# Kernel optimization log

Measured on AMD Instinct MI355X. Metric: run time of the kernel, lower is better.

The kernel has to match this reference:

```python
import jax, jax.numpy as jnp
import numpy as np
from jax import lax

B, T, D = 1, 2048, 2048
H, KVH, HD = 16, 4, 128
BETA = 0.9
ROPE_BASE = 10000.0


def _causal_prefix_ema(x, beta):
    # x: (B, T, D); m_t = beta * m_{t-1} + (1 - beta) * x_t, m_{-1} = 0
    def step(m, xt):
        m = beta * m + (1.0 - beta) * xt
        return m, m
    _, ys = lax.scan(step, jnp.zeros_like(x[:, 0]), jnp.swapaxes(x, 0, 1))
    return jnp.swapaxes(ys, 0, 1)


def _rotate_half(x):
    x1, x2 = jnp.split(x, 2, axis=-1)
    return jnp.concatenate([-x2, x1], axis=-1)


def _rope_cos_sin(t, hd, dtype):
    inv_freq = 1.0 / (ROPE_BASE ** (jnp.arange(0, hd, 2, dtype=jnp.float32) / hd))
    freqs = jnp.arange(t, dtype=jnp.float32)[:, None] * inv_freq[None, :]  # (T, HD/2)
    emb = jnp.concatenate([freqs, freqs], axis=-1)  # (T, HD)
    return jnp.cos(emb).astype(dtype)[None, None], jnp.sin(emb).astype(dtype)[None, None]


def setup_inputs() -> dict:
    key = jax.random.key(0)
    ks = jax.random.split(key, 8)
    std = 0.02
    return {
        "hidden_states": jax.random.normal(ks[0], (B, T, D), jnp.float32),
        "Wq": jax.random.normal(ks[1], (D, H * HD), jnp.float32) * std,
        "Wk": jax.random.normal(ks[2], (D, KVH * HD), jnp.float32) * std,
        "Wv": jax.random.normal(ks[3], (D, KVH * HD), jnp.float32) * std,
        "Wo": jax.random.normal(ks[4], (H * HD, D), jnp.float32) * std,
        "Wr1": jax.random.normal(ks[5], (D, D // 2), jnp.float32) * std,
        "br1": jnp.zeros((D // 2,), jnp.float32),
        "Wr2": jax.random.normal(ks[6], (D // 2, 2), jnp.float32) * std,
        "br2": jnp.zeros((2,), jnp.float32),
    }


def reference(hidden_states, Wq, Wk, Wv, Wo, Wr1, br1, Wr2, br2):
    b, t, d = hidden_states.shape
    q = hidden_states @ Wq  # (B, T, H*HD)

    # multi-level memories: l1 = raw, l2 = causal prefix EMA
    l2 = _causal_prefix_ema(hidden_states, BETA)

    # router MLP on q + softmax over levels
    h = jax.nn.silu(q @ Wr1 + br1)
    lam = jax.nn.softmax(h @ Wr2 + br2, axis=-1)  # (B, T, 2)
    fused = lam[..., 0:1] * hidden_states + lam[..., 1:2] * l2

    # shape to heads
    q_s = q.reshape(b, t, H, HD).transpose(0, 2, 1, 3)                 # (B, H, T, HD)
    k_s = (fused @ Wk).reshape(b, t, KVH, HD).transpose(0, 2, 1, 3)    # (B, KVH, T, HD)
    v_s = (fused @ Wv).reshape(b, t, KVH, HD).transpose(0, 2, 1, 3)

    # RoPE
    cos, sin = _rope_cos_sin(t, HD, q_s.dtype)
    q_s = q_s * cos + _rotate_half(q_s) * sin
    k_s = k_s * cos + _rotate_half(k_s) * sin

    # repeat kv for GQA
    n_rep = H // KVH
    k_s = jnp.repeat(k_s, n_rep, axis=1)
    v_s = jnp.repeat(v_s, n_rep, axis=1)

    # causal SDPA
    scale = 1.0 / jnp.sqrt(jnp.asarray(HD, q_s.dtype))
    scores = jnp.einsum("bhqd,bhkd->bhqk", q_s, k_s) * scale
    causal = jnp.tril(jnp.ones((t, t), dtype=bool))
    scores = jnp.where(causal[None, None], scores, jnp.finfo(scores.dtype).min)
    attn = jax.nn.softmax(scores, axis=-1)
    out = jnp.einsum("bhqk,bhkd->bhqd", attn, v_s)  # (B, H, T, HD)

    out = out.transpose(0, 2, 1, 3).reshape(b, t, H * HD)
    return out @ Wo
```

## Files before the change

### kernel.cpp

```cpp
#include <hip/hip_runtime.h>
#include <hip/hip_bf16.h>

#define T_SEQ 2048
#define D_MODEL 2048
#define NH 16
#define NKVH 4
#define HD 128

typedef __attribute__((ext_vector_type(8))) short bf16x8;
typedef __attribute__((ext_vector_type(4))) float f32x4;

static __device__ __forceinline__ short f32_to_bf16(float f) {
    unsigned u = __float_as_uint(f);
    u += 0x7fffu + ((u >> 16) & 1u);
    return (short)(u >> 16);
}
static __device__ __forceinline__ float bf16_to_f32(short s) {
    return __uint_as_float(((unsigned)(unsigned short)s) << 16);
}
static __device__ __forceinline__ void gl_to_lds16(const void* g, void* l) {
    __builtin_amdgcn_global_load_lds(
        (const __attribute__((address_space(1))) unsigned int*)g,
        (__attribute__((address_space(3))) unsigned int*)l, 16, 0, 0);
}

template<int BM>
__global__ __launch_bounds__(256) void gemm_bt_kernel(
    const short* __restrict__ A, const short* __restrict__ Bt,
    float* __restrict__ Cf, short* __restrict__ Cb,
    int M, int N, int K, const float* __restrict__ bias, int act)
{
    constexpr int NI = (BM == 128) ? 4 : 2;
    constexpr int ACH = BM / 32;
    __shared__ short Alds[2][BM * 64];
    __shared__ short Blds[2][128 * 64];

    const int tid = threadIdx.x;
    const int wave = tid >> 6, lane = tid & 63;
    const int l16 = lane & 15, quad = lane >> 4;
    const int wm = (BM == 128) ? (wave >> 1) * 64 : 0;
    const int wn = (BM == 128) ? (wave & 1) * 64 : wave * 32;
    const int m0 = blockIdx.y * BM, n0 = blockIdx.x * 128;
    const int niter = K >> 6;

    f32x4 acc[4][NI] = {};

    #pragma unroll
    for (int p = 0; p < ACH; ++p) {
        int li = p * 256 + tid;
        int row = li >> 3, sc = li & 7;
        gl_to_lds16(A + (size_t)(m0 + row) * K + ((sc ^ (row & 7)) * 8),
                    &Alds[0][(size_t)(p * 256 + wave * 64) * 8]);
    }
    #pragma unroll
    for (int p = 0; p < 4; ++p) {
        int li = p * 256 + tid;
        int row = li >> 3, sc = li & 7;
        gl_to_lds16(Bt + (size_t)(n0 + row) * K + ((sc ^ (row & 7)) * 8),
                    &Blds[0][(size_t)(p * 256 + wave * 64) * 8]);
    }

    for (int t = 0; t < niter; ++t) {
        asm volatile("s_waitcnt vmcnt(0)\n\ts_barrier" ::: "memory");

        if (t + 1 < niter) {
            int k1 = (t + 1) << 6;
            int nb = (t + 1) & 1;
            #pragma unroll
            for (int p = 0; p < ACH; ++p) {
                int li = p * 256 + tid;
                int row = li >> 3, sc = li & 7;
                gl_to_lds16(A + (size_t)(m0 + row) * K + k1 + ((sc ^ (row & 7)) * 8),
                            &Alds[nb][(size_t)(p * 256 + wave * 64) * 8]);
            }
            #pragma unroll
            for (int p = 0; p < 4; ++p) {
                int li = p * 256 + tid;
                int row = li >> 3, sc = li & 7;
                gl_to_lds16(Bt + (size_t)(n0 + row) * K + k1 + ((sc ^ (row & 7)) * 8),
                            &Blds[nb][(size_t)(p * 256 + wave * 64) * 8]);
            }
        }

        const short* Ab = Alds[t & 1];
        const short* Bb = Blds[t & 1];
        #pragma unroll
        for (int kk = 0; kk < 2; ++kk) {
            bf16x8 a[4], b[NI];
            #pragma unroll
            for (int i = 0; i < 4; ++i)
                a[i] = *(const bf16x8*)
                    &Ab[(size_t)(wm + i * 16 + l16) * 64 + (((kk * 4 + quad) ^ (l16 & 7)) * 8)];
            #pragma unroll
            for (int i = 0; i < NI; ++i)
                b[i] = *(const bf16x8*)
                    &Bb[(size_t)(wn + i * 16 + l16) * 64 + (((kk * 4 + quad) ^ (l16 & 7)) * 8)];
            #pragma unroll
            for (int mi = 0; mi < 4; ++mi)
                #pragma unroll
                for (int ni = 0; ni < NI; ++ni)
                    acc[mi][ni] = __builtin_amdgcn_mfma_f32_16x16x32_bf16(
                        a[mi], b[ni], acc[mi][ni], 0, 0, 0);
        }
    }

    #pragma unroll
    for (int mi = 0; mi < 4; ++mi) {
        #pragma unroll
        for (int ni = 0; ni < NI; ++ni) {
            int col = n0 + wn + ni * 16 + l16;
            float bv = bias ? bias[col] : 0.0f;
            #pragma unroll
            for (int r = 0; r < 4; ++r) {
                int row = m0 + wm + mi * 16 + quad * 4 + r;
                float x = acc[mi][ni][r] + bv;
                if (act) x = x / (1.0f + __expf(-x));
                size_t o = (size_t)row * N + col;
                if (Cf) Cf[o] = x;
                if (Cb) Cb[o] = f32_to_bf16(x);
            }
        }
    }
}

__global__ __launch_bounds__(256) void transpose_all_kernel(
    const float* __restrict__ Wq, const float* __restrict__ Wk,
    const float* __restrict__ Wv, const float* __restrict__ Wr1,
    const float* __restrict__ Wo, short* __restrict__ Wq_t,
    short* __restrict__ Wkv_t, short* __restrict__ Wr1_t,
    short* __restrict__ Wo_t)
{
    __shared__ float tile[32][33];
    int bx = blockIdx.x;
    const float* src; short* dst; int ld, cb;
    if (bx < 64)       { src = Wq;  dst = Wq_t;  ld = 2048; cb = bx; }
    else if (bx < 80)  { src = Wk;  dst = Wkv_t; ld = 512;  cb = bx - 64; }
    else if (bx < 96)  { src = Wv;  dst = Wkv_t + (size_t)512 * 2048; ld = 512; cb = bx - 80; }
    else if (bx < 128) { src = Wr1; dst = Wr1_t; ld = 1024; cb = bx - 96; }
    else               { src = Wo;  dst = Wo_t;  ld = 2048; cb = bx - 128; }
    int c0 = cb * 32, r0 = blockIdx.y * 32;
    int t = threadIdx.x;
    int r = t >> 3, c4 = (t & 7) * 4;
    float4 v = *(const float4*)&src[(size_t)(r0 + r) * ld + c0 + c4];
    tile[r][c4 + 0] = v.x; tile[r][c4 + 1] = v.y;
    tile[r][c4 + 2] = v.z; tile[r][c4 + 3] = v.w;
    __syncthreads();
    short o[4];
    #pragma unroll
    for (int j = 0; j < 4; ++j) o[j] = f32_to_bf16(tile[c4 + j][r]);
    *(uint2*)&dst[(size_t)(c0 + r) * 2048 + r0 + c4] = *(const uint2*)o;
}

__global__ __launch_bounds__(256) void transpose_bf_kernel(
    const short* __restrict__ src, int ld, short* __restrict__ dst, int ldd)
{
    __shared__ float tile[32][33];
    int r0 = blockIdx.y * 32, c0 = blockIdx.x * 32;
    int x = threadIdx.x & 31, y = threadIdx.x >> 5;
    #pragma unroll
    for (int i = 0; i < 4; ++i)
        tile[y + i * 8][x] = bf16_to_f32(src[(size_t)(r0 + y + i * 8) * ld + c0 + x]);
    __syncthreads();
    #pragma unroll
    for (int i = 0; i < 4; ++i)
        dst[(size_t)(c0 + y + i * 8) * ldd + r0 + x] = f32_to_bf16(tile[x][y + i * 8]);
}

__global__ void conv_bf16_kernel(const float* __restrict__ src, short* __restrict__ dst)
{
    int i = blockIdx.x * blockDim.x + threadIdx.x;
    float4 v = ((const float4*)src)[i];
    short o[4] = {f32_to_bf16(v.x), f32_to_bf16(v.y), f32_to_bf16(v.z), f32_to_bf16(v.w)};
    *(uint2*)(dst + (size_t)i * 4) = *(const uint2*)o;
}

__global__ __launch_bounds__(256) void ema_kernel(const float* __restrict__ hs,
                                                  float* __restrict__ l2)
{
    int d = blockIdx.y * 256 + threadIdx.x;
    int t0 = blockIdx.x * 128;
    int ts = t0 - 192; if (ts < 0) ts = 0;
    float m = 0.0f;
    for (int tb = ts; tb < t0; tb += 16) {
        float buf[16];
        #pragma unroll
        for (int j = 0; j < 16; ++j) buf[j] = hs[(size_t)(tb + j) * D_MODEL + d];
        #pragma unroll
        for (int j = 0; j < 16; ++j) m = 0.9f * m + 0.1f * buf[j];
    }
    for (int tb = t0; tb < t0 + 128; tb += 16) {
        float buf[16];
        #pragma unroll
        for (int j = 0; j < 16; ++j) buf[j] = hs[(size_t)(tb + j) * D_MODEL + d];
        #pragma unroll
        for (int j = 0; j < 16; ++j) { m = 0.9f * m + 0.1f * buf[j]; buf[j] = m; }
        #pragma unroll
        for (int j = 0; j < 16; ++j) l2[(size_t)(tb + j) * D_MODEL + d] = buf[j];
    }
}

__global__ __launch_bounds__(64) void lam_kernel(
    const short* __restrict__ h, const float* __restrict__ Wr2,
    const float* __restrict__ br2, float* __restrict__ lam)
{
    int t = blockIdx.x;
    int lane = threadIdx.x;
    float z0 = 0.0f, z1 = 0.0f;
    for (int i = lane; i < 1024; i += 64) {
        float hv = bf16_to_f32(h[(size_t)t * 1024 + i]);
        z0 += hv * Wr2[i * 2 + 0];
        z1 += hv * Wr2[i * 2 + 1];
    }
    #pragma unroll
    for (int off = 1; off < 64; off <<= 1) {
        z0 += __shfl_xor(z0, off);
        z1 += __shfl_xor(z1, off);
    }
    if (lane == 0) {
        z0 += br2[0]; z1 += br2[1];
        float mx = fmaxf(z0, z1);
        float e0 = expf(z0 - mx), e1 = expf(z1 - mx);
        float inv = 1.0f / (e0 + e1);
        lam[t * 2 + 0] = e0 * inv;
        lam[t * 2 + 1] = e1 * inv;
    }
}

__global__ void fuse_kernel(const float* __restrict__ hs, const float* __restrict__ l2,
                            const float* __restrict__ lam, short* __restrict__ fused)
{
    int idx = blockIdx.x * blockDim.x + threadIdx.x;
    int t = idx >> 9;
    float a0 = lam[t * 2 + 0], a1 = lam[t * 2 + 1];
    float4 a = ((const float4*)hs)[idx];
    float4 b = ((const float4*)l2)[idx];
    short o[4] = {f32_to_bf16(a0 * a.x + a1 * b.x), f32_to_bf16(a0 * a.y + a1 * b.y),
                  f32_to_bf16(a0 * a.z + a1 * b.z), f32_to_bf16(a0 * a.w + a1 * b.w)};
    *(uint2*)(fused + (size_t)idx * 4) = *(const uint2*)o;
}

__global__ void rope_q_kernel(const short* __restrict__ q, short* __restrict__ qr)
{
    int idx = blockIdx.x * blockDim.x + threadIdx.x;
    int d = idx & 63;
    int h = (idx >> 6) & 15;
    int t = idx >> 10;
    float fr = (float)t * __expf(-(float)d * 0.14391156831212787f);
    float s, c;
    sincosf(fr, &s, &c);
    const float sc = 0.08838834764831845f;
    const short* src = q + (size_t)t * D_MODEL + h * HD;
    float x1 = bf16_to_f32(src[d]) * sc, x2 = bf16_to_f32(src[d + 64]) * sc;
    short* dst = qr + ((size_t)h * T_SEQ + t) * HD;
    dst[d]      = f32_to_bf16(x1 * c - x2 * s);
    dst[d + 64] = f32_to_bf16(x2 * c + x1 * s);
}

__global__ void rope_k_kernel(const short* __restrict__ kv, short* __restrict__ kr)
{
    int idx = blockIdx.x * blockDim.x + threadIdx.x;
    int d = idx & 63;
    int kh = (idx >> 6) & 3;
    int t = idx >> 8;
    float fr = (float)t * __expf(-(float)d * 0.14391156831212787f);
    float s, c;
    sincosf(fr, &s, &c);
    const short* src = kv + (size_t)t * 1024 + kh * HD;
    float x1 = bf16_to_f32(src[d]), x2 = bf16_to_f32(src[d + 64]);
    short* dst = kr + ((size_t)kh * T_SEQ + t) * HD;
    dst[d]      = f32_to_bf16(x1 * c - x2 * s);
    dst[d + 64] = f32_to_bf16(x2 * c + x1 * s);
}

__global__ __launch_bounds__(256, 1) void attn_kernel(
    const short* __restrict__ Qr, const short* __restrict__ Kr,
    const short* __restrict__ Vt, short* __restrict__ Out)
{
    const int pi = blockIdx.x;
    const int h = blockIdx.y;
    const int kvh = h >> 2;
    const int tid = threadIdx.x;
    const int wave = tid >> 6, lane = tid & 63;
    const int l16 = lane & 15, quad = lane >> 4;

    __shared__ short Klds[2][128 * 128];
    __shared__ short Vlds[2][128 * 128];
    __shared__ short Plds[4][16][136];

    const short* kbase = Kr + (size_t)kvh * T_SEQ * HD;
    const short* vbase = Vt + (size_t)kvh * HD * T_SEQ;

    for (int ph = 0; ph < 2; ++ph) {
        const int qt = ph ? (31 - pi) : pi;
        const int qbase = qt * 64 + wave * 16;
        const int n = (qt * 64 + 191) >> 7;

        bf16x8 qf[4];
        {
            const short* qrow = Qr + ((size_t)h * T_SEQ + qbase + l16) * HD;
            #pragma unroll
            for (int kc = 0; kc < 4; ++kc)
                qf[kc] = *(const bf16x8*)&qrow[kc * 32 + quad * 8];
        }
        f32x4 o[8] = {};
        float lsum[4] = {0.0f, 0.0f, 0.0f, 0.0f};

        __syncthreads();

        {
            const short* ks = kbase;
            #pragma unroll
            for (int p = 0; p < 8; ++p) {
                int li = p * 256 + tid;
                int row = li >> 4, gs = (li & 15) ^ (row & 15);
                gl_to_lds16(ks + (size_t)row * HD + gs * 8,
                            &Klds[0][(size_t)(p * 256 + wave * 64) * 8]);
            }
            #pragma unroll
            for (int p = 0; p < 8; ++p) {
                int li = p * 256 + tid;
                int row = li >> 4, gs = (li & 15) ^ (row & 15);
                gl_to_lds16(vbase + (size_t)row * T_SEQ + gs * 8,
                            &Vlds[0][(size_t)(p * 256 + wave * 64) * 8]);
            }
        }

        for (int t = 0; t < n; ++t) {
            asm volatile("s_waitcnt vmcnt(0)\n\ts_barrier" ::: "memory");

            if (t + 1 < n) {
                int kv1 = (t + 1) << 7;
                int nb = (t + 1) & 1;
                const short* ks = kbase + (size_t)kv1 * HD;
                #pragma unroll
                for (int p = 0; p < 8; ++p) {
                    int li = p * 256 + tid;
                    int row = li >> 4, gs = (li & 15) ^ (row & 15);
                    gl_to_lds16(ks + (size_t)row * HD + gs * 8,
                                &Klds[nb][(size_t)(p * 256 + wave * 64) * 8]);
                }
                #pragma unroll
                for (int p = 0; p < 8; ++p) {
                    int li = p * 256 + tid;
                    int row = li >> 4, gs = (li & 15) ^ (row & 15);
                    gl_to_lds16(vbase + (size_t)row * T_SEQ + kv1 + gs * 8,
                                &Vlds[nb][(size_t)(p * 256 + wave * 64) * 8]);
                }
            }

            const short* Kb = Klds[t & 1];
            const short* Vb = Vlds[t & 1];

            f32x4 s[8];
            #pragma unroll
            for (int ni = 0; ni < 8; ++ni) s[ni] = (f32x4){0, 0, 0, 0};
            #pragma unroll
            for (int ni = 0; ni < 8; ++ni)
                #pragma unroll
                for (int kc = 0; kc < 4; ++kc) {
                    bf16x8 b = *(const bf16x8*)
                        &Kb[(size_t)(ni * 16 + l16) * 128 + (((kc * 4 + quad) ^ l16) * 8)];
                    s[ni] = __builtin_amdgcn_mfma_f32_16x16x32_bf16(qf[kc], b, s[ni], 0, 0, 0);
                }

            if (t == n - 1) {
                int kvg0 = t << 7;
                #pragma unroll
                for (int ni = 0; ni < 8; ++ni) {
                    int kvg = kvg0 + ni * 16 + l16;
                    #pragma unroll
                    for (int r = 0; r < 4; ++r) {
                        int qg = qbase + quad * 4 + r;
                        float p = (kvg <= qg) ? __expf(s[ni][r]) : 0.0f;
                        lsum[r] += p;
                        Plds[wave][quad * 4 + r][ni * 16 + l16] = f32_to_bf16(p);
                    }
                }
            } else {
                #pragma unroll
                for (int ni = 0; ni < 8; ++ni)
                    #pragma unroll
                    for (int r = 0; r < 4; ++r) {
                        float p = __expf(s[ni][r]);
                        lsum[r] += p;
                        Plds[wave][quad * 4 + r][ni * 16 + l16] = f32_to_bf16(p);
                    }
            }
            asm volatile("s_waitcnt lgkmcnt(0)" ::: "memory");

            #pragma unroll
            for (int kc = 0; kc < 4; ++kc) {
                bf16x8 pa = *(const bf16x8*)&Plds[wave][l16][kc * 32 + quad * 8];
                #pragma unroll
                for (int d8 = 0; d8 < 8; ++d8) {
                    bf16x8 b = *(const bf16x8*)
                        &Vb[(size_t)(d8 * 16 + l16) * 128 + (((kc * 4 + quad) ^ l16) * 8)];
                    o[d8] = __builtin_amdgcn_mfma_f32_16x16x32_bf16(pa, b, o[d8], 0, 0, 0);
                }
            }
        }

        #pragma unroll
        for (int r = 0; r < 4; ++r) {
            #pragma unroll
            for (int off = 1; off < 16; off <<= 1)
                lsum[r] += __shfl_xor(lsum[r], off);
            lsum[r] = 1.0f / lsum[r];
        }
        #pragma unroll
        for (int d8 = 0; d8 < 8; ++d8)
            #pragma unroll
            for (int r = 0; r < 4; ++r) {
                int row = qbase + quad * 4 + r;
                Out[(size_t)row * D_MODEL + h * HD + d8 * 16 + l16] =
                    f32_to_bf16(o[d8][r] * lsum[r]);
            }
    }
}

extern "C" void kernel_launch(void* const* d_in, const int* in_sizes, int n_in,
                              void* d_out, int out_size, void* d_ws, size_t ws_size,
                              hipStream_t stream)
{
    const float* hs  = (const float*)d_in[0];
    const float* Wq  = (const float*)d_in[1];
    const float* Wk  = (const float*)d_in[2];
    const float* Wv  = (const float*)d_in[3];
    const float* Wo  = (const float*)d_in[4];
    const float* Wr1 = (const float*)d_in[5];
    const float* br1 = (const float*)d_in[6];
    const float* Wr2 = (const float*)d_in[7];
    const float* br2 = (const float*)d_in[8];
    float* out = (float*)d_out;

    char* w = (char*)d_ws;
    const size_t MB = 1u << 20;
    float* l2_f     = (float*)(w + 0 * MB);
    short* hs_bf    = (short*)(w + 16 * MB);
    short* Wq_t     = (short*)(w + 24 * MB);
    short* Wkv_t    = (short*)(w + 32 * MB);
    short* Wr1_t    = (short*)(w + 36 * MB);
    short* Wo_t     = (short*)(w + 40 * MB);
    short* q_bf     = (short*)(w + 48 * MB);
    short* h_bf     = (short*)(w + 56 * MB);
    short* fused_bf = (short*)(w + 60 * MB);
    short* kv_bf    = (short*)(w + 68 * MB);
    short* qr       = (short*)(w + 72 * MB);
    short* kr       = (short*)(w + 80 * MB);
    short* vr       = (short*)(w + 82 * MB);
    float* lam_f    = (float*)(w + 84 * MB);
    short* attn_bf  = hs_bf;

    transpose_all_kernel<<<dim3(192, 64), 256, 0, stream>>>(
        Wq, Wk, Wv, Wr1, Wo, Wq_t, Wkv_t, Wr1_t, Wo_t);
    conv_bf16_kernel<<<(T_SEQ * D_MODEL / 4) / 256, 256, 0, stream>>>(hs, hs_bf);

    ema_kernel<<<dim3(T_SEQ / 128, D_MODEL / 256), 256, 0, stream>>>(hs, l2_f);

    gemm_bt_kernel<128><<<dim3(16, 16), 256, 0, stream>>>(
        hs_bf, Wq_t, nullptr, q_bf, 2048, 2048, 2048, nullptr, 0);

    gemm_bt_kernel<64><<<dim3(8, 32), 256, 0, stream>>>(
        q_bf, Wr1_t, nullptr, h_bf, 2048, 1024, 2048, br1, 1);

    lam_kernel<<<T_SEQ, 64, 0, stream>>>(h_bf, Wr2, br2, lam_f);

    fuse_kernel<<<(T_SEQ * D_MODEL / 4) / 256, 256, 0, stream>>>(hs, l2_f, lam_f, fused_bf);

    gemm_bt_kernel<64><<<dim3(8, 32), 256, 0, stream>>>(
        fused_bf, Wkv_t, nullptr, kv_bf, 2048, 1024, 2048, nullptr, 0);

    rope_q_kernel<<<(T_SEQ * NH * 64) / 256, 256, 0, stream>>>(q_bf, qr);
    rope_k_kernel<<<(T_SEQ * NKVH * 64) / 256, 256, 0, stream>>>(kv_bf, kr);
    transpose_bf_kernel<<<dim3(16, 64), 256, 0, stream>>>(kv_bf + 512, 1024, vr, 2048);

    attn_kernel<<<dim3(16, NH), 256, 0, stream>>>(qr, kr, vr, attn_bf);

    gemm_bt_kernel<128><<<dim3(16, 16), 256, 0, stream>>>(
        attn_bf, Wo_t, out, nullptr, 2048, 2048, 2048, nullptr, 0);
}
```

Baseline: 349.5 us.

## Fuse RoPE, router head, bf16 conversion and V transpose into GEMM epilogues; retile attention

The Q GEMM epilogue now applies RoPE and the attention scale directly, and the KV GEMM epilogue writes rotated K and transposed V, which removes the separate rope and transpose kernels. The router GEMM epilogue applies SiLU and the Wr2 projection, accumulating logits with atomics, so the h buffer and lam kernel go away and the softmax over levels moves into fuse_kernel. The EMA kernel also emits the bf16 copy of hidden states, replacing conv_bf16. Attention waves are re-split into 2x2 query/key halves sharing a P tile, with block barriers and a cross-wave row-sum reduction through LDS; this adds synchronisation and atomic nondeterminism in exchange for fewer launches and less memory traffic.

New measurement: 361.0 us. +3.3%, slower.

```diff
diff --git a/kernel.cpp b/kernel.cpp
--- a/kernel.cpp
+++ b/kernel.cpp
@@ -10,6 +10,9 @@
 typedef __attribute__((ext_vector_type(8))) short bf16x8;
 typedef __attribute__((ext_vector_type(4))) float f32x4;
 
+#define ROPE_C 0.14391156831212787f
+#define QSCALE 0.08838834764831845f
+
 static __device__ __forceinline__ short f32_to_bf16(float f) {
     unsigned u = __float_as_uint(f);
     u += 0x7fffu + ((u >> 16) & 1u);
@@ -24,11 +27,12 @@
         (__attribute__((address_space(3))) unsigned int*)l, 16, 0, 0);
 }
 
-template<int BM>
+template<int BM, int EPI>
 __global__ __launch_bounds__(256) void gemm_bt_kernel(
     const short* __restrict__ A, const short* __restrict__ Bt,
-    float* __restrict__ Cf, short* __restrict__ Cb,
-    int M, int N, int K, const float* __restrict__ bias, int act)
+    float* __restrict__ Cf, short* __restrict__ O0, short* __restrict__ O1,
+    int M, int N, int K, const float* __restrict__ bias,
+    const float* __restrict__ Wr2, float* __restrict__ logits)
 {
     constexpr int NI = (BM == 128) ? 4 : 2;
     constexpr int ACH = BM / 32;
@@ -43,6 +47,14 @@
     const int m0 = blockIdx.y * BM, n0 = blockIdx.x * 128;
     const int niter = K >> 6;
 
+    int coln[NI];
+    #pragma unroll
+    for (int i = 0; i < NI; ++i) {
+        if (EPI == 1)      coln[i] = (wave & 1) * 32 + (i & 1) * 16 + (i >> 1) * 64;
+        else if (EPI == 2) coln[i] = (wave >> 1) * 32 + (wave & 1) * 16 + i * 64;
+        else               coln[i] = wn + i * 16;
+    }
+
     f32x4 acc[4][NI] = {};
 
     #pragma unroll
@@ -92,9 +104,11 @@
                 a[i] = *(const bf16x8*)
                     &Ab[(size_t)(wm + i * 16 + l16) * 64 + (((kk * 4 + quad) ^ (l16 & 7)) * 8)];
             #pragma unroll
-            for (int i = 0; i < NI; ++i)
+            for (int i = 0; i < NI; ++i) {
+                int row = coln[i] + l16;
                 b[i] = *(const bf16x8*)
-                    &Bb[(size_t)(wn + i * 16 + l16) * 64 + (((kk * 4 + quad) ^ (l16 & 7)) * 8)];
+                    &Bb[(size_t)row * 64 + (((kk * 4 + quad) ^ (row & 7)) * 8)];
+            }
             #pragma unroll
             for (int mi = 0; mi < 4; ++mi)
                 #pragma unroll
@@ -104,22 +118,95 @@
         }
     }
 
-    #pragma unroll
-    for (int mi = 0; mi < 4; ++mi) {
-        #pragma unroll
-        for (int ni = 0; ni < NI; ++ni) {
-            int col = n0 + wn + ni * 16 + l16;
-            float bv = bias ? bias[col] : 0.0f;
+    if (EPI == 0) {
+        #pragma unroll
+        for (int mi = 0; mi < 4; ++mi)
+            #pragma unroll
+            for (int ni = 0; ni < NI; ++ni) {
+                int col = n0 + coln[ni] + l16;
+                #pragma unroll
+                for (int r = 0; r < 4; ++r) {
+                    int row = m0 + wm + mi * 16 + quad * 4 + r;
+                    Cf[(size_t)row * N + col] = acc[mi][ni][r];
+                }
+            }
+    } else if (EPI == 1) {
+        const int h = blockIdx.x;
+        #pragma unroll
+        for (int mi = 0; mi < 4; ++mi)
             #pragma unroll
             for (int r = 0; r < 4; ++r) {
-                int row = m0 + wm + mi * 16 + quad * 4 + r;
-                float x = acc[mi][ni][r] + bv;
-                if (act) x = x / (1.0f + __expf(-x));
-                size_t o = (size_t)row * N + col;
-                if (Cf) Cf[o] = x;
-                if (Cb) Cb[o] = f32_to_bf16(x);
-            }
-        }
+                int t = m0 + wm + mi * 16 + quad * 4 + r;
+                #pragma unroll
+                for (int ip = 0; ip < 2; ++ip) {
+                    int d = coln[ip] + l16;
+                    float x1 = acc[mi][ip][r], x2 = acc[mi][ip + 2][r];
+                    O0[(size_t)t * D_MODEL + h * HD + d]      = f32_to_bf16(x1);
+                    O0[(size_t)t * D_MODEL + h * HD + d + 64] = f32_to_bf16(x2);
+                    float fr = (float)t * __expf(-(float)d * ROPE_C);
+                    float s, c;
+                    sincosf(fr, &s, &c);
+                    size_t o = ((size_t)h * T_SEQ + t) * HD + d;
+                    O1[o]      = f32_to_bf16((x1 * c - x2 * s) * QSCALE);
+                    O1[o + 64] = f32_to_bf16((x2 * c + x1 * s) * QSCALE);
+                }
+            }
+    } else if (EPI == 2) {
+        const int hn = blockIdx.x;
+        if (hn < 4) {
+            #pragma unroll
+            for (int mi = 0; mi < 4; ++mi)
+                #pragma unroll
+                for (int r = 0; r < 4; ++r) {
+                    int t = m0 + mi * 16 + quad * 4 + r;
+                    int d = coln[0] + l16;
+                    float x1 = acc[mi][0][r], x2 = acc[mi][1][r];
+                    float fr = (float)t * __expf(-(float)d * ROPE_C);
+                    float s, c;
+                    sincosf(fr, &s, &c);
+                    size_t o = ((size_t)hn * T_SEQ + t) * HD + d;
+                    O0[o]      = f32_to_bf16(x1 * c - x2 * s);
+                    O0[o + 64] = f32_to_bf16(x2 * c + x1 * s);
+                }
+        } else {
+            int vh = hn - 4;
+            #pragma unroll
+            for (int mi = 0; mi < 4; ++mi)
+                #pragma unroll
+                for (int ni = 0; ni < 2; ++ni) {
+                    int d = coln[ni] + l16;
+                    int t0 = m0 + mi * 16 + quad * 4;
+                    short pk[4];
+                    #pragma unroll
+                    for (int r = 0; r < 4; ++r) pk[r] = f32_to_bf16(acc[mi][ni][r]);
+                    *(uint2*)&O1[((size_t)vh * HD + d) * T_SEQ + t0] = *(const uint2*)pk;
+                }
+        }
+    } else if (EPI == 3) {
+        #pragma unroll
+        for (int mi = 0; mi < 4; ++mi)
+            #pragma unroll
+            for (int r = 0; r < 4; ++r) {
+                float z0 = 0.0f, z1 = 0.0f;
+                #pragma unroll
+                for (int ni = 0; ni < 2; ++ni) {
+                    int col = n0 + coln[ni] + l16;
+                    float x = acc[mi][ni][r] + bias[col];
+                    x = x / (1.0f + __expf(-x));
+                    z0 += x * Wr2[col * 2 + 0];
+                    z1 += x * Wr2[col * 2 + 1];
+                }
+                #pragma unroll
+                for (int off = 1; off < 16; off <<= 1) {
+                    z0 += __shfl_xor(z0, off);
+                    z1 += __shfl_xor(z1, off);
+                }
+                if (l16 == 0) {
+                    int row = m0 + mi * 16 + quad * 4 + r;
+                    atomicAdd(&logits[row * 2 + 0], z0);
+                    atomicAdd(&logits[row * 2 + 1], z1);
+                }
+            }
     }
 }
 
@@ -151,31 +238,9 @@
     *(uint2*)&dst[(size_t)(c0 + r) * 2048 + r0 + c4] = *(const uint2*)o;
 }
 
-__global__ __launch_bounds__(256) void transpose_bf_kernel(
-    const short* __restrict__ src, int ld, short* __restrict__ dst, int ldd)
-{
-    __shared__ float tile[32][33];
-    int r0 = blockIdx.y * 32, c0 = blockIdx.x * 32;
-    int x = threadIdx.x & 31, y = threadIdx.x >> 5;
-    #pragma unroll
-    for (int i = 0; i < 4; ++i)
-        tile[y + i * 8][x] = bf16_to_f32(src[(size_t)(r0 + y + i * 8) * ld + c0 + x]);
-    __syncthreads();
-    #pragma unroll
-    for (int i = 0; i < 4; ++i)
-        dst[(size_t)(c0 + y + i * 8) * ldd + r0 + x] = f32_to_bf16(tile[x][y + i * 8]);
-}
-
-__global__ void conv_bf16_kernel(const float* __restrict__ src, short* __restrict__ dst)
-{
-    int i = blockIdx.x * blockDim.x + threadIdx.x;
-    float4 v = ((const float4*)src)[i];
-    short o[4] = {f32_to_bf16(v.x), f32_to_bf16(v.y), f32_to_bf16(v.z), f32_to_bf16(v.w)};
-    *(uint2*)(dst + (size_t)i * 4) = *(const uint2*)o;
-}
-
 __global__ __launch_bounds__(256) void ema_kernel(const float* __restrict__ hs,
-                                                  float* __restrict__ l2)
+                                                  float* __restrict__ l2,
+                                                  short* __restrict__ hs_b)
 {
     int d = blockIdx.y * 256 + threadIdx.x;
     int t0 = blockIdx.x * 128;
@@ -193,83 +258,31 @@
         #pragma unroll
         for (int j = 0; j < 16; ++j) buf[j] = hs[(size_t)(tb + j) * D_MODEL + d];
         #pragma unroll
+        for (int j = 0; j < 16; ++j) hs_b[(size_t)(tb + j) * D_MODEL + d] = f32_to_bf16(buf[j]);
+        #pragma unroll
         for (int j = 0; j < 16; ++j) { m = 0.9f * m + 0.1f * buf[j]; buf[j] = m; }
         #pragma unroll
         for (int j = 0; j < 16; ++j) l2[(size_t)(tb + j) * D_MODEL + d] = buf[j];
     }
 }
 
-__global__ __launch_bounds__(64) void lam_kernel(
-    const short* __restrict__ h, const float* __restrict__ Wr2,
-    const float* __restrict__ br2, float* __restrict__ lam)
-{
-    int t = blockIdx.x;
-    int lane = threadIdx.x;
-    float z0 = 0.0f, z1 = 0.0f;
-    for (int i = lane; i < 1024; i += 64) {
-        float hv = bf16_to_f32(h[(size_t)t * 1024 + i]);
-        z0 += hv * Wr2[i * 2 + 0];
-        z1 += hv * Wr2[i * 2 + 1];
-    }
-    #pragma unroll
-    for (int off = 1; off < 64; off <<= 1) {
-        z0 += __shfl_xor(z0, off);
-        z1 += __shfl_xor(z1, off);
-    }
-    if (lane == 0) {
-        z0 += br2[0]; z1 += br2[1];
-        float mx = fmaxf(z0, z1);
-        float e0 = expf(z0 - mx), e1 = expf(z1 - mx);
-        float inv = 1.0f / (e0 + e1);
-        lam[t * 2 + 0] = e0 * inv;
-        lam[t * 2 + 1] = e1 * inv;
-    }
-}
-
 __global__ void fuse_kernel(const float* __restrict__ hs, const float* __restrict__ l2,
-                            const float* __restrict__ lam, short* __restrict__ fused)
+                            const float* __restrict__ logits, const float* __restrict__ br2,
+                            short* __restrict__ fused)
 {
     int idx = blockIdx.x * blockDim.x + threadIdx.x;
     int t = idx >> 9;
-    float a0 = lam[t * 2 + 0], a1 = lam[t * 2 + 1];
+    float z0 = logits[t * 2 + 0] + br2[0];
+    float z1 = logits[t * 2 + 1] + br2[1];
+    float mx = fmaxf(z0, z1);
+    float e0 = __expf(z0 - mx), e1 = __expf(z1 - mx);
+    float inv = 1.0f / (e0 + e1);
+    float a0 = e0 * inv, a1 = e1 * inv;
     float4 a = ((const float4*)hs)[idx];
     float4 b = ((const float4*)l2)[idx];
     short o[4] = {f32_to_bf16(a0 * a.x + a1 * b.x), f32_to_bf16(a0 * a.y + a1 * b.y),
                   f32_to_bf16(a0 * a.z + a1 * b.z), f32_to_bf16(a0 * a.w + a1 * b.w)};
     *(uint2*)(fused + (size_t)idx * 4) = *(const uint2*)o;
-}
-
-__global__ void rope_q_kernel(const short* __restrict__ q, short* __restrict__ qr)
-{
-    int idx = blockIdx.x * blockDim.x + threadIdx.x;
-    int d = idx & 63;
-    int h = (idx >> 6) & 15;
-    int t = idx >> 10;
-    float fr = (float)t * __expf(-(float)d * 0.14391156831212787f);
-    float s, c;
-    sincosf(fr, &s, &c);
-    const float sc = 0.08838834764831845f;
-    const short* src = q + (size_t)t * D_MODEL + h * HD;
-    float x1 = bf16_to_f32(src[d]) * sc, x2 = bf16_to_f32(src[d + 64]) * sc;
-    short* dst = qr + ((size_t)h * T_SEQ + t) * HD;
-    dst[d]      = f32_to_bf16(x1 * c - x2 * s);
-    dst[d + 64] = f32_to_bf16(x2 * c + x1 * s);
-}
-
-__global__ void rope_k_kernel(const short* __restrict__ kv, short* __restrict__ kr)
-{
-    int idx = blockIdx.x * blockDim.x + threadIdx.x;
-    int d = idx & 63;
-    int kh = (idx >> 6) & 3;
-    int t = idx >> 8;
-    float fr = (float)t * __expf(-(float)d * 0.14391156831212787f);
-    float s, c;
-    sincosf(fr, &s, &c);
-    const short* src = kv + (size_t)t * 1024 + kh * HD;
-    float x1 = bf16_to_f32(src[d]), x2 = bf16_to_f32(src[d + 64]);
-    short* dst = kr + ((size_t)kh * T_SEQ + t) * HD;
-    dst[d]      = f32_to_bf16(x1 * c - x2 * s);
-    dst[d + 64] = f32_to_bf16(x2 * c + x1 * s);
 }
 
 __global__ __launch_bounds__(256, 1) void attn_kernel(
@@ -282,47 +295,48 @@
     const int tid = threadIdx.x;
     const int wave = tid >> 6, lane = tid & 63;
     const int l16 = lane & 15, quad = lane >> 4;
+    const int qh = wave >> 1;
+    const int kh2 = wave & 1;
 
     __shared__ short Klds[2][128 * 128];
     __shared__ short Vlds[2][128 * 128];
-    __shared__ short Plds[4][16][136];
+    __shared__ short Plds[64][136];
+    __shared__ float lred[2][64];
 
     const short* kbase = Kr + (size_t)kvh * T_SEQ * HD;
     const short* vbase = Vt + (size_t)kvh * HD * T_SEQ;
 
     for (int ph = 0; ph < 2; ++ph) {
         const int qt = ph ? (31 - pi) : pi;
-        const int qbase = qt * 64 + wave * 16;
-        const int n = (qt * 64 + 191) >> 7;
-
-        bf16x8 qf[4];
-        {
-            const short* qrow = Qr + ((size_t)h * T_SEQ + qbase + l16) * HD;
+        const int qblk = qt * 64;
+        const int n = (qblk + 191) >> 7;
+
+        bf16x8 qf[2][4];
+        #pragma unroll
+        for (int qs = 0; qs < 2; ++qs) {
+            const short* qrow = Qr + ((size_t)h * T_SEQ + qblk + qh * 32 + qs * 16 + l16) * HD;
             #pragma unroll
             for (int kc = 0; kc < 4; ++kc)
-                qf[kc] = *(const bf16x8*)&qrow[kc * 32 + quad * 8];
-        }
-        f32x4 o[8] = {};
-        float lsum[4] = {0.0f, 0.0f, 0.0f, 0.0f};
+                qf[qs][kc] = *(const bf16x8*)&qrow[kc * 32 + quad * 8];
+        }
+        f32x4 o[2][4] = {};
+        float lsum[2][4] = {};
 
         __syncthreads();
 
-        {
-            const short* ks = kbase;
-            #pragma unroll
-            for (int p = 0; p < 8; ++p) {
-                int li = p * 256 + tid;
-                int row = li >> 4, gs = (li & 15) ^ (row & 15);
-                gl_to_lds16(ks + (size_t)row * HD + gs * 8,
-                            &Klds[0][(size_t)(p * 256 + wave * 64) * 8]);
-            }
-            #pragma unroll
-            for (int p = 0; p < 8; ++p) {
-                int li = p * 256 + tid;
-                int row = li >> 4, gs = (li & 15) ^ (row & 15);
-                gl_to_lds16(vbase + (size_t)row * T_SEQ + gs * 8,
-                            &Vlds[0][(size_t)(p * 256 + wave * 64) * 8]);
-            }
+        #pragma unroll
+        for (int p = 0; p < 8; ++p) {
+            int li = p * 256 + tid;
+            int row = li >> 4, gs = (li & 15) ^ (row & 15);
+            gl_to_lds16(kbase + (size_t)row * HD + gs * 8,
+                        &Klds[0][(size_t)(p * 256 + wave * 64) * 8]);
+        }
+        #pragma unroll
+        for (int p = 0; p < 8; ++p) {
+            int li = p * 256 + tid;
+            int row = li >> 4, gs = (li & 15) ^ (row & 15);
+            gl_to_lds16(vbase + (size_t)row * T_SEQ + gs * 8,
+                        &Vlds[0][(size_t)(p * 256 + wave * 64) * 8]);
         }
 
         for (int t = 0; t < n; ++t) {
@@ -351,70 +365,108 @@
             const short* Kb = Klds[t & 1];
             const short* Vb = Vlds[t & 1];
 
-            f32x4 s[8];
-            #pragma unroll
-            for (int ni = 0; ni < 8; ++ni) s[ni] = (f32x4){0, 0, 0, 0};
-            #pragma unroll
-            for (int ni = 0; ni < 8; ++ni)
+            f32x4 s[2][4];
+            #pragma unroll
+            for (int qs = 0; qs < 2; ++qs)
+                #pragma unroll
+                for (int ks = 0; ks < 4; ++ks) s[qs][ks] = (f32x4){0, 0, 0, 0};
+            #pragma unroll
+            for (int ks = 0; ks < 4; ++ks)
                 #pragma unroll
                 for (int kc = 0; kc < 4; ++kc) {
+                    int row = kh2 * 64 + ks * 16 + l16;
                     bf16x8 b = *(const bf16x8*)
-                        &Kb[(size_t)(ni * 16 + l16) * 128 + (((kc * 4 + quad) ^ l16) * 8)];
-                    s[ni] = __builtin_amdgcn_mfma_f32_16x16x32_bf16(qf[kc], b, s[ni], 0, 0, 0);
+                        &Kb[(size_t)row * 128 + (((kc * 4 + quad) ^ l16) * 8)];
+                    #pragma unroll
+                    for (int qs = 0; qs < 2; ++qs)
+                        s[qs][ks] = __builtin_amdgcn_mfma_f32_16x16x32_bf16(
+                            qf[qs][kc], b, s[qs][ks], 0, 0, 0);
                 }
 
             if (t == n - 1) {
-                int kvg0 = t << 7;
-                #pragma unroll
-                for (int ni = 0; ni < 8; ++ni) {
-                    int kvg = kvg0 + ni * 16 + l16;
+                #pragma unroll
+                for (int ks = 0; ks < 4; ++ks) {
+                    int kvg = (t << 7) + kh2 * 64 + ks * 16 + l16;
                     #pragma unroll
-                    for (int r = 0; r < 4; ++r) {
-                        int qg = qbase + quad * 4 + r;
-                        float p = (kvg <= qg) ? __expf(s[ni][r]) : 0.0f;
-                        lsum[r] += p;
-                        Plds[wave][quad * 4 + r][ni * 16 + l16] = f32_to_bf16(p);
-                    }
+                    for (int qs = 0; qs < 2; ++qs)
+                        #pragma unroll
+                        for (int r = 0; r < 4; ++r) {
+                            int qg = qblk + qh * 32 + qs * 16 + quad * 4 + r;
+                            float p = (kvg <= qg) ? __expf(s[qs][ks][r]) : 0.0f;
+                            lsum[qs][r] += p;
+                            Plds[qh * 32 + qs * 16 + quad * 4 + r][kh2 * 64 + ks * 16 + l16]
+                                = f32_to_bf16(p);
+                        }
                 }
             } else {
                 #pragma unroll
-                for (int ni = 0; ni < 8; ++ni)
+                for (int ks = 0; ks < 4; ++ks)
                     #pragma unroll
-                    for (int r = 0; r < 4; ++r) {
-                        float p = __expf(s[ni][r]);
-                        lsum[r] += p;
-                        Plds[wave][quad * 4 + r][ni * 16 + l16] = f32_to_bf16(p);
-                    }
-            }
-            asm volatile("s_waitcnt lgkmcnt(0)" ::: "memory");
+                    for (int qs = 0; qs < 2; ++qs)
+                        #pragma unroll
+                        for (int r = 0; r < 4; ++r) {
+                            float p = __expf(s[qs][ks][r]);
+                            lsum[qs][r] += p;
+                            Plds[qh * 32 + qs * 16 + quad * 4 + r][kh2 * 64 + ks * 16 + l16]
+                                = f32_to_bf16(p);
+                        }
+            }
+            asm volatile("s_waitcnt lgkmcnt(0)\n\ts_barrier" ::: "memory");
 
             #pragma unroll
             for (int kc = 0; kc < 4; ++kc) {
-                bf16x8 pa = *(const bf16x8*)&Plds[wave][l16][kc * 32 + quad * 8];
-                #pragma unroll
-                for (int d8 = 0; d8 < 8; ++d8) {
+                bf16x8 pa[2];
+                #pragma unroll
+                for (int qs = 0; qs < 2; ++qs)
+                    pa[qs] = *(const bf16x8*)
+                        &Plds[qh * 32 + qs * 16 + l16][kc * 32 + quad * 8];
+                #pragma unroll
+                for (int ds = 0; ds < 4; ++ds) {
+                    int vrow = kh2 * 64 + ds * 16 + l16;
                     bf16x8 b = *(const bf16x8*)
-                        &Vb[(size_t)(d8 * 16 + l16) * 128 + (((kc * 4 + quad) ^ l16) * 8)];
-                    o[d8] = __builtin_amdgcn_mfma_f32_16x16x32_bf16(pa, b, o[d8], 0, 0, 0);
-                }
-            }
-        }
-
-        #pragma unroll
-        for (int r = 0; r < 4; ++r) {
-            #pragma unroll
-            for (int off = 1; off < 16; off <<= 1)
-                lsum[r] += __shfl_xor(lsum[r], off);
-            lsum[r] = 1.0f / lsum[r];
-        }
-        #pragma unroll
-        for (int d8 = 0; d8 < 8; ++d8)
+                        &Vb[(size_t)vrow * 128 + (((kc * 4 + quad) ^ l16) * 8)];
+                    #pragma unroll
+                    for (int qs = 0; qs < 2; ++qs)
+                        o[qs][ds] = __builtin_amdgcn_mfma_f32_16x16x32_bf16(
+                            pa[qs], b, o[qs][ds], 0, 0, 0);
+                }
+            }
+        }
+
+        #pragma unroll
+        for (int qs = 0; qs < 2; ++qs)
             #pragma unroll
             for (int r = 0; r < 4; ++r) {
-                int row = qbase + quad * 4 + r;
-                Out[(size_t)row * D_MODEL + h * HD + d8 * 16 + l16] =
-                    f32_to_bf16(o[d8][r] * lsum[r]);
-            }
+                #pragma unroll
+                for (int off = 1; off < 16; off <<= 1)
+                    lsum[qs][r] += __shfl_xor(lsum[qs][r], off);
+            }
+        if (l16 == 0) {
+            #pragma unroll
+            for (int qs = 0; qs < 2; ++qs)
+                #pragma unroll
+                for (int r = 0; r < 4; ++r)
+                    lred[kh2][qh * 32 + qs * 16 + quad * 4 + r] = lsum[qs][r];
+        }
+        asm volatile("s_waitcnt lgkmcnt(0)\n\ts_barrier" ::: "memory");
+        float inv[2][4];
+        #pragma unroll
+        for (int qs = 0; qs < 2; ++qs)
+            #pragma unroll
+            for (int r = 0; r < 4; ++r)
+                inv[qs][r] = 1.0f / (lsum[qs][r] +
+                                     lred[kh2 ^ 1][qh * 32 + qs * 16 + quad * 4 + r]);
+        #pragma unroll
+        for (int qs = 0; qs < 2; ++qs)
+            #pragma unroll
+            for (int ds = 0; ds < 4; ++ds)
+                #pragma unroll
+                for (int r = 0; r < 4; ++r) {
+                    int row = qblk + qh * 32 + qs * 16 + quad * 4 + r;
+                    int d = kh2 * 64 + ds * 16 + l16;
+                    Out[(size_t)row * D_MODEL + h * HD + d] =
+                        f32_to_bf16(o[qs][ds][r] * inv[qs][r]);
+                }
     }
 }
 
@@ -442,40 +494,34 @@
     short* Wr1_t    = (short*)(w + 36 * MB);
     short* Wo_t     = (short*)(w + 40 * MB);
     short* q_bf     = (short*)(w + 48 * MB);
-    short* h_bf     = (short*)(w + 56 * MB);
     short* fused_bf = (short*)(w + 60 * MB);
-    short* kv_bf    = (short*)(w + 68 * MB);
     short* qr       = (short*)(w + 72 * MB);
     short* kr       = (short*)(w + 80 * MB);
     short* vr       = (short*)(w + 82 * MB);
     float* lam_f    = (float*)(w + 84 * MB);
     short* attn_bf  = hs_bf;
 
+    hipMemsetAsync(lam_f, 0, T_SEQ * 2 * sizeof(float), stream);
+
     transpose_all_kernel<<<dim3(192, 64), 256, 0, stream>>>(
         Wq, Wk, Wv, Wr1, Wo, Wq_t, Wkv_t, Wr1_t, Wo_t);
-    conv_bf16_kernel<<<(T_SEQ * D_MODEL / 4) / 256, 256, 0, stream>>>(hs, hs_bf);
-
-    ema_kernel<<<dim3(T_SEQ / 128, D_MODEL / 256), 256, 0, stream>>>(hs, l2_f);
-
-    gemm_bt_kernel<128><<<dim3(16, 16), 256, 0, stream>>>(
-        hs_bf, Wq_t, nullptr, q_bf, 2048, 2048, 2048, nullptr, 0);
-
-    gemm_bt_kernel<64><<<dim3(8, 32), 256, 0, stream>>>(
-        q_bf, Wr1_t, nullptr, h_bf, 2048, 1024, 2048, br1, 1);
-
-    lam_kernel<<<T_SEQ, 64, 0, stream>>>(h_bf, Wr2, br2, lam_f);
-
-    fuse_kernel<<<(T_SEQ * D_MODEL / 4) / 256, 256, 0, stream>>>(hs, l2_f, lam_f, fused_bf);
-
-    gemm_bt_kernel<64><<<dim3(8, 32), 256, 0, stream>>>(
-        fused_bf, Wkv_t, nullptr, kv_bf, 2048, 1024, 2048, nullptr, 0);
-
-    rope_q_kernel<<<(T_SEQ * NH * 64) / 256, 256, 0, stream>>>(q_bf, qr);
-    rope_k_kernel<<<(T_SEQ * NKVH * 64) / 256, 256, 0, stream>>>(kv_bf, kr);
-    transpose_bf_kernel<<<dim3(16, 64), 256, 0, stream>>>(kv_bf + 512, 1024, vr, 2048);
+
+    ema_kernel<<<dim3(T_SEQ / 128, D_MODEL / 256), 256, 0, stream>>>(hs, l2_f, hs_bf);
+
+    gemm_bt_kernel<128, 1><<<dim3(16, 16), 256, 0, stream>>>(
+        hs_bf, Wq_t, nullptr, q_bf, qr, 2048, 2048, 2048, nullptr, nullptr, nullptr);
+
+    gemm_bt_kernel<64, 3><<<dim3(8, 32), 256, 0, stream>>>(
+        q_bf, Wr1_t, nullptr, nullptr, nullptr, 2048, 1024, 2048, br1, Wr2, lam_f);
+
+    fuse_kernel<<<(T_SEQ * D_MODEL / 4) / 256, 256, 0, stream>>>(
+        hs, l2_f, lam_f, br2, fused_bf);
+
+    gemm_bt_kernel<64, 2><<<dim3(8, 32), 256, 0, stream>>>(
+        fused_bf, Wkv_t, nullptr, kr, vr, 2048, 1024, 2048, nullptr, nullptr, nullptr);
 
     attn_kernel<<<dim3(16, NH), 256, 0, stream>>>(qr, kr, vr, attn_bf);
 
-    gemm_bt_kernel<128><<<dim3(16, 16), 256, 0, stream>>>(
-        attn_bf, Wo_t, out, nullptr, 2048, 2048, 2048, nullptr, 0);
-}
+    gemm_bt_kernel<128, 0><<<dim3(16, 16), 256, 0, stream>>>(
+        attn_bf, Wo_t, out, nullptr, nullptr, 2048, 2048, 2048, nullptr, nullptr, nullptr);
+}
```

## Retile GEMMs to 64-row blocks and fold bf16 conversion into EMA

Applied to the files above, without the earlier changes.

The GEMM kernel now uses a fixed 64-row M tile with a templated N tile, and requests two blocks per CU through launch bounds. Launch grids are doubled so that more workgroups cover the 256 CUs. The separate hidden-state bf16 conversion kernel is removed, and that conversion now happens inside the EMA kernel, which already reads hs. A no-op multiply by 1.0 is also added to the attention output accumulator. Smaller tiles lower per-block reuse but increase occupancy and parallelism, and the EMA kernel still writes the overlapping warmup rows only once.

Result: faster. 315.8 us (-9.6%).

```diff
diff --git a/kernel.cpp b/kernel.cpp
--- a/kernel.cpp
+++ b/kernel.cpp
@@ -24,36 +24,35 @@
         (__attribute__((address_space(3))) unsigned int*)l, 16, 0, 0);
 }
 
-template<int BM>
-__global__ __launch_bounds__(256) void gemm_bt_kernel(
+template<int BN>
+__global__ __launch_bounds__(256, 2) void gemm_bt_kernel(
     const short* __restrict__ A, const short* __restrict__ Bt,
     float* __restrict__ Cf, short* __restrict__ Cb,
     int M, int N, int K, const float* __restrict__ bias, int act)
 {
-    constexpr int NI = (BM == 128) ? 4 : 2;
-    constexpr int ACH = BM / 32;
-    __shared__ short Alds[2][BM * 64];
-    __shared__ short Blds[2][128 * 64];
+    constexpr int NI = BN / 64;
+    constexpr int BCH = BN / 32;
+    __shared__ short Alds[2][64 * 64];
+    __shared__ short Blds[2][BN * 64];
 
     const int tid = threadIdx.x;
     const int wave = tid >> 6, lane = tid & 63;
     const int l16 = lane & 15, quad = lane >> 4;
-    const int wm = (BM == 128) ? (wave >> 1) * 64 : 0;
-    const int wn = (BM == 128) ? (wave & 1) * 64 : wave * 32;
-    const int m0 = blockIdx.y * BM, n0 = blockIdx.x * 128;
+    const int wn = wave * (BN / 4);
+    const int m0 = blockIdx.y * 64, n0 = blockIdx.x * BN;
     const int niter = K >> 6;
 
     f32x4 acc[4][NI] = {};
 
     #pragma unroll
-    for (int p = 0; p < ACH; ++p) {
+    for (int p = 0; p < 2; ++p) {
         int li = p * 256 + tid;
         int row = li >> 3, sc = li & 7;
         gl_to_lds16(A + (size_t)(m0 + row) * K + ((sc ^ (row & 7)) * 8),
                     &Alds[0][(size_t)(p * 256 + wave * 64) * 8]);
     }
     #pragma unroll
-    for (int p = 0; p < 4; ++p) {
+    for (int p = 0; p < BCH; ++p) {
         int li = p * 256 + tid;
         int row = li >> 3, sc = li & 7;
         gl_to_lds16(Bt + (size_t)(n0 + row) * K + ((sc ^ (row & 7)) * 8),
@@ -67,14 +66,14 @@
             int k1 = (t + 1) << 6;
             int nb = (t + 1) & 1;
             #pragma unroll
-            for (int p = 0; p < ACH; ++p) {
+            for (int p = 0; p < 2; ++p) {
                 int li = p * 256 + tid;
                 int row = li >> 3, sc = li & 7;
                 gl_to_lds16(A + (size_t)(m0 + row) * K + k1 + ((sc ^ (row & 7)) * 8),
                             &Alds[nb][(size_t)(p * 256 + wave * 64) * 8]);
             }
             #pragma unroll
-            for (int p = 0; p < 4; ++p) {
+            for (int p = 0; p < BCH; ++p) {
                 int li = p * 256 + tid;
                 int row = li >> 3, sc = li & 7;
                 gl_to_lds16(Bt + (size_t)(n0 + row) * K + k1 + ((sc ^ (row & 7)) * 8),
@@ -90,7 +89,7 @@
             #pragma unroll
             for (int i = 0; i < 4; ++i)
                 a[i] = *(const bf16x8*)
-                    &Ab[(size_t)(wm + i * 16 + l16) * 64 + (((kk * 4 + quad) ^ (l16 & 7)) * 8)];
+                    &Ab[(size_t)(i * 16 + l16) * 64 + (((kk * 4 + quad) ^ (l16 & 7)) * 8)];
             #pragma unroll
             for (int i = 0; i < NI; ++i)
                 b[i] = *(const bf16x8*)
@@ -112,7 +111,7 @@
             float bv = bias ? bias[col] : 0.0f;
             #pragma unroll
             for (int r = 0; r < 4; ++r) {
-                int row = m0 + wm + mi * 16 + quad * 4 + r;
+                int row = m0 + mi * 16 + quad * 4 + r;
                 float x = acc[mi][ni][r] + bv;
                 if (act) x = x / (1.0f + __expf(-x));
                 size_t o = (size_t)row * N + col;
@@ -166,16 +165,9 @@
         dst[(size_t)(c0 + y + i * 8) * ldd + r0 + x] = f32_to_bf16(tile[x][y + i * 8]);
 }
 
-__global__ void conv_bf16_kernel(const float* __restrict__ src, short* __restrict__ dst)
-{
-    int i = blockIdx.x * blockDim.x + threadIdx.x;
-    float4 v = ((const float4*)src)[i];
-    short o[4] = {f32_to_bf16(v.x), f32_to_bf16(v.y), f32_to_bf16(v.z), f32_to_bf16(v.w)};
-    *(uint2*)(dst + (size_t)i * 4) = *(const uint2*)o;
-}
-
 __global__ __launch_bounds__(256) void ema_kernel(const float* __restrict__ hs,
-                                                  float* __restrict__ l2)
+                                                  float* __restrict__ l2,
+                                                  short* __restrict__ hs_b)
 {
     int d = blockIdx.y * 256 + threadIdx.x;
     int t0 = blockIdx.x * 128;
@@ -192,6 +184,8 @@
         float buf[16];
         #pragma unroll
         for (int j = 0; j < 16; ++j) buf[j] = hs[(size_t)(tb + j) * D_MODEL + d];
+        #pragma unroll
+        for (int j = 0; j < 16; ++j) hs_b[(size_t)(tb + j) * D_MODEL + d] = f32_to_bf16(buf[j]);
         #pragma unroll
         for (int j = 0; j < 16; ++j) { m = 0.9f * m + 0.1f * buf[j]; buf[j] = m; }
         #pragma unroll
@@ -388,6 +382,10 @@
             }
             asm volatile("s_waitcnt lgkmcnt(0)" ::: "memory");
 
+            #pragma unroll
+            for (int d8 = 0; d8 < 8; ++d8)
+                #pragma unroll
+                for (int r = 0; r < 4; ++r) o[d8][r] *= 1.0f;
             #pragma unroll
             for (int kc = 0; kc < 4; ++kc) {
                 bf16x8 pa = *(const bf16x8*)&Plds[wave][l16][kc * 32 + quad * 8];
@@ -453,21 +451,20 @@
 
     transpose_all_kernel<<<dim3(192, 64), 256, 0, stream>>>(
         Wq, Wk, Wv, Wr1, Wo, Wq_t, Wkv_t, Wr1_t, Wo_t);
-    conv_bf16_kernel<<<(T_SEQ * D_MODEL / 4) / 256, 256, 0, stream>>>(hs, hs_bf);
-
-    ema_kernel<<<dim3(T_SEQ / 128, D_MODEL / 256), 256, 0, stream>>>(hs, l2_f);
-
-    gemm_bt_kernel<128><<<dim3(16, 16), 256, 0, stream>>>(
+
+    ema_kernel<<<dim3(T_SEQ / 128, D_MODEL / 256), 256, 0, stream>>>(hs, l2_f, hs_bf);
+
+    gemm_bt_kernel<128><<<dim3(16, 32), 256, 0, stream>>>(
         hs_bf, Wq_t, nullptr, q_bf, 2048, 2048, 2048, nullptr, 0);
 
-    gemm_bt_kernel<64><<<dim3(8, 32), 256, 0, stream>>>(
+    gemm_bt_kernel<64><<<dim3(16, 32), 256, 0, stream>>>(
         q_bf, Wr1_t, nullptr, h_bf, 2048, 1024, 2048, br1, 1);
 
     lam_kernel<<<T_SEQ, 64, 0, stream>>>(h_bf, Wr2, br2, lam_f);
 
     fuse_kernel<<<(T_SEQ * D_MODEL / 4) / 256, 256, 0, stream>>>(hs, l2_f, lam_f, fused_bf);
 
-    gemm_bt_kernel<64><<<dim3(8, 32), 256, 0, stream>>>(
+    gemm_bt_kernel<64><<<dim3(16, 32), 256, 0, stream>>>(
         fused_bf, Wkv_t, nullptr, kv_bf, 2048, 1024, 2048, nullptr, 0);
 
     rope_q_kernel<<<(T_SEQ * NH * 64) / 256, 256, 0, stream>>>(q_bf, qr);
@@ -476,6 +473,6 @@
 
     attn_kernel<<<dim3(16, NH), 256, 0, stream>>>(qr, kr, vr, attn_bf);
 
-    gemm_bt_kernel<128><<<dim3(16, 16), 256, 0, stream>>>(
+    gemm_bt_kernel<128><<<dim3(16, 32), 256, 0, stream>>>(
         attn_bf, Wo_t, out, nullptr, 2048, 2048, 2048, nullptr, 0);
 }
```
